# Kernel optimization log

Measured on AMD Instinct MI355X. Metric: run time of the kernel, lower is better.

## Reference

```python
import jax, jax.numpy as jnp
import numpy as np

B, H, W, C = 4, 64, 64, 512
DQK = C // 8


def setup_inputs() -> dict:
    key = jax.random.key(0)
    k1, k2, k3, k4 = jax.random.split(key, 4)
    x = jax.random.normal(k1, (B, H, W, C), dtype=jnp.float32)
    kernel_f = jax.random.normal(k2, (1, 1, C, DQK), dtype=jnp.float32) * 0.02
    kernel_g = jax.random.normal(k3, (1, 1, C, DQK), dtype=jnp.float32) * 0.02
    kernel_h = jax.random.normal(k4, (1, 1, C, C), dtype=jnp.float32) * 0.02
    gamma = jnp.ones((1,), dtype=jnp.float32)  # nonzero so attention branch contributes
    return {"x": x, "kernel_f": kernel_f, "kernel_g": kernel_g,
            "kernel_h": kernel_h, "gamma": gamma}


def reference(x, kernel_f, kernel_g, kernel_h, gamma):
    b, h, w, c = x.shape
    n = h * w
    xt = x.reshape(b, n, c)  # 1x1 conv == per-pixel matmul
    f = jnp.einsum('bnc,cd->bnd', xt, kernel_f[0, 0])       # [b,n,dqk]
    g = jnp.einsum('bnc,cd->bnd', xt, kernel_g[0, 0])       # [b,n,dqk]
    v = jnp.einsum('bnc,cd->bnd', xt, kernel_h[0, 0])       # [b,n,c]
    s = jnp.einsum('bid,bjd->bij', f, g)                    # [b,n,n] = f @ g^T
    beta = jax.nn.softmax(s, axis=-1)
    out = jnp.einsum('bij,bjc->bic', beta, v)               # [b,n,c]
    out = out.reshape(b, h, w, c)
    return gamma * out + x
```

## Files before the change

### kernel.cpp

```cpp
#include <hip/hip_runtime.h>


typedef __bf16 bf16x8 __attribute__((ext_vector_type(8)));
typedef __bf16 bf16x2 __attribute__((ext_vector_type(2)));
typedef float f32x4 __attribute__((ext_vector_type(4)));
typedef unsigned int u32x4 __attribute__((ext_vector_type(4)));
typedef unsigned int u32;

#define L2E 1.4426950408889634f

__device__ __forceinline__ unsigned short f2bf(float f) {
    unsigned int u = __builtin_bit_cast(unsigned int, f);
    u += 0x7fffu + ((u >> 16) & 1u);
    return (unsigned short)(u >> 16);
}
__device__ __forceinline__ u32 cvtpk(float a, float b) {
    bf16x2 t; t[0] = (__bf16)a; t[1] = (__bf16)b;
    return __builtin_bit_cast(u32, t);
}
__device__ __forceinline__ bf16x8 ld8(const void* p) {
    u32x4 u = *reinterpret_cast<const u32x4*>(p);
    return __builtin_bit_cast(bf16x8, u);
}
__device__ __forceinline__ bf16x8 ldx(const float* p) {
    float4 a = *reinterpret_cast<const float4*>(p);
    float4 b = *reinterpret_cast<const float4*>(p + 4);
    u32x4 r;
    r.x = cvtpk(a.x, a.y); r.y = cvtpk(a.z, a.w);
    r.z = cvtpk(b.x, b.y); r.w = cvtpk(b.z, b.w);
    return __builtin_bit_cast(bf16x8, r);
}
__device__ __forceinline__ f32x4 mfma16(bf16x8 a, bf16x8 b, f32x4 c) {
    return __builtin_amdgcn_mfma_f32_16x16x32_bf16(a, b, c, 0, 0, 0);
}
__device__ __forceinline__ void gl2lds16(const void* g, void* l) {
    __builtin_amdgcn_global_load_lds(
        (const __attribute__((address_space(1))) u32*)g,
        (__attribute__((address_space(3))) u32*)l, 16, 0, 0);
}

__global__ __launch_bounds__(256) void cvt_w_all(const float* __restrict__ kf,
                                                 const float* __restrict__ kg,
                                                 const float* __restrict__ kh,
                                                 unsigned short* __restrict__ wst) {
    int idx = blockIdx.x * 256 + threadIdx.x;
    int j = idx & 7;
    int gi = idx >> 3;
    int c = gi % 640;
    int sq = gi / 640;
    int k = (sq >> 2) * 32 + (sq & 3) * 8 + j;
    float v;
    if (c < 64)       v = kf[k * 64 + c] * L2E;
    else if (c < 128) v = kg[k * 64 + (c - 64)];
    else              v = kh[k * 512 + (c - 128)];
    wst[idx] = f2bf(v);
}

__global__ __launch_bounds__(256, 2) void proj_k(const float* __restrict__ x,
                                                 const unsigned short* __restrict__ wst,
                                                 unsigned short* __restrict__ fq,
                                                 unsigned short* __restrict__ kst,
                                                 unsigned short* __restrict__ vst) {
    __shared__ __align__(16) unsigned char Wl[2][20480];
    __shared__ unsigned short Tl[64][72];

    int m0 = blockIdx.x * 64;
    int grp = blockIdx.y;
    int tid = threadIdx.x;
    int w = tid >> 6, l = tid & 63, g = l >> 4, i = l & 15;

    const char* wsrc = (const char*)wst + (size_t)w * 10240 + (size_t)grp * 5120 + l * 16;

#pragma unroll
    for (int s5 = 0; s5 < 5; s5++)
        gl2lds16(wsrc + s5 * 1024, &Wl[0][w * 5120 + s5 * 1024]);

    const float* xrow = x + (size_t)(m0 + 16 * w + i) * 512 + g * 8;
    bf16x8 af[16];
#pragma unroll
    for (int k = 0; k < 16; k++) af[k] = ldx(xrow + 32 * k);

    f32x4 acc[5][4];
#pragma unroll
    for (int t = 0; t < 5; t++)
#pragma unroll
        for (int cf = 0; cf < 4; cf++) acc[t][cf] = f32x4{0, 0, 0, 0};

    int rdoff = g * 5120 + i * 16;

#pragma unroll
    for (int q = 0; q < 16; q++) {
        __syncthreads();
        if (q < 15) {
            const char* src = wsrc + (size_t)(q + 1) * 40960;
#pragma unroll
            for (int s5 = 0; s5 < 5; s5++)
                gl2lds16(src + s5 * 1024, &Wl[(q + 1) & 1][w * 5120 + s5 * 1024]);
        }
        const unsigned char* Wb = &Wl[q & 1][0];
        __builtin_amdgcn_s_setprio(1);
#pragma unroll
        for (int t = 0; t < 5; t++)
#pragma unroll
            for (int cf = 0; cf < 4; cf++) {
                bf16x8 bb = ld8(Wb + rdoff + (t * 64 + 16 * cf) * 16);
                acc[t][cf] = mfma16(af[q], bb, acc[t][cf]);
            }
        __builtin_amdgcn_s_setprio(0);
    }

    int batch = m0 >> 12;
    int kt = (m0 & 4095) >> 6;
    unsigned short* kbase = kst + (size_t)batch * 262144 + (size_t)kt * 4096;
    unsigned short* vbase = vst + (size_t)batch * 2097152 + (size_t)kt * 32768;

#pragma unroll
    for (int t = 0; t < 5; t++) {
        if (grp == 0 && t == 0) {
#pragma unroll
            for (int cf = 0; cf < 4; cf++)
#pragma unroll
                for (int r = 0; r < 4; r++)
                    fq[(size_t)(m0 + 16 * w + 4 * g + r) * 64 + 16 * cf + i] =
                        f2bf(acc[t][cf][r]);
        } else {
            __syncthreads();
#pragma unroll
            for (int cf = 0; cf < 4; cf++) {
                ushort4 v4;
                v4.x = f2bf(acc[t][cf][0]); v4.y = f2bf(acc[t][cf][1]);
                v4.z = f2bf(acc[t][cf][2]); v4.w = f2bf(acc[t][cf][3]);
                *reinterpret_cast<ushort4*>(&Tl[16 * cf + i][16 * w + 4 * g]) = v4;
            }
            __syncthreads();
            if (grp == 0 && t == 1) {
#pragma unroll
                for (int ch = tid; ch < 512; ch += 256) {
                    int jf2 = ch >> 7, ks = (ch >> 6) & 1, l2 = ch & 63;
                    int g2 = l2 >> 4, i2 = l2 & 15;
                    ushort4 o0, o1;
                    o0.x = Tl[ks * 32 + 8 * g2 + 0][16 * jf2 + i2];
                    o0.y = Tl[ks * 32 + 8 * g2 + 1][16 * jf2 + i2];
                    o0.z = Tl[ks * 32 + 8 * g2 + 2][16 * jf2 + i2];
                    o0.w = Tl[ks * 32 + 8 * g2 + 3][16 * jf2 + i2];
                    o1.x = Tl[ks * 32 + 8 * g2 + 4][16 * jf2 + i2];
                    o1.y = Tl[ks * 32 + 8 * g2 + 5][16 * jf2 + i2];
                    o1.z = Tl[ks * 32 + 8 * g2 + 6][16 * jf2 + i2];
                    o1.w = Tl[ks * 32 + 8 * g2 + 7][16 * jf2 + i2];
                    unsigned short* dst = kbase + (size_t)(jf2 * 1024 + ks * 512 + l2 * 8);
                    *reinterpret_cast<ushort4*>(dst)     = o0;
                    *reinterpret_cast<ushort4*>(dst + 4) = o1;
                }
            } else {
                int n0 = (grp == 0) ? (t - 2) * 64 : 192 + t * 64;
#pragma unroll
                for (int ch = tid; ch < 512; ch += 256) {
                    int cc = ch >> 7, ks = (ch >> 6) & 1, l2 = ch & 63;
                    int g2 = l2 >> 4, i2 = l2 & 15;
                    int row = cc * 16 + i2;
                    int jb = 32 * ks + 4 * g2;
                    ushort4 o0, o1;
                    o0.x = Tl[row][jb + 0];  o0.y = Tl[row][jb + 1];
                    o0.z = Tl[row][jb + 2];  o0.w = Tl[row][jb + 3];
                    o1.x = Tl[row][jb + 16]; o1.y = Tl[row][jb + 17];
                    o1.z = Tl[row][jb + 18]; o1.w = Tl[row][jb + 19];
                    int c16 = (n0 >> 4) + cc;
                    unsigned short* dst = vbase + (size_t)(c16 * 1024 + ks * 512 + l2 * 8);
                    *reinterpret_cast<ushort4*>(dst)     = o0;
                    *reinterpret_cast<ushort4*>(dst + 4) = o1;
                }
            }
        }
    }
}

__global__ __launch_bounds__(512, 2) void attn_k(const unsigned short* __restrict__ fq,
                                                 const unsigned short* __restrict__ kst,
                                                 const unsigned short* __restrict__ vst,
                                                 const float* __restrict__ x,
                                                 const float* __restrict__ gamma,
                                                 float* __restrict__ out) {
    __shared__ __align__(16) unsigned char Pl[4][8192];
    __shared__ float l_lds[64];

    int bid = blockIdx.x;
    int xcd = bid & 7;
    int batch = xcd >> 1;
    int qidx = ((xcd & 1) << 5) | (bid >> 3);
    int q0 = qidx * 64;

    int tid = threadIdx.x;
    int w = tid >> 6, l = tid & 63, g = l >> 4, i = l & 15;
    int jf = w >> 1, qfh = w & 1;

    if (tid < 64) l_lds[tid] = 0.0f;

    const unsigned short* fqb = fq + (size_t)batch * 4096 * 64;
    const char* kb = (const char*)kst + (size_t)batch * 524288;
    const char* vb = (const char*)vst + (size_t)batch * 4194304;

    bf16x8 aQ[2][2];
#pragma unroll
    for (int qf_l = 0; qf_l < 2; qf_l++)
#pragma unroll
        for (int ks = 0; ks < 2; ks++)
            aQ[qf_l][ks] = ld8(fqb + (size_t)(q0 + 16 * (2 * qfh + qf_l) + i) * 64 +
                               ks * 32 + g * 8);

    f32x4 acc[4][4];
#pragma unroll
    for (int a = 0; a < 4; a++)
#pragma unroll
        for (int b = 0; b < 4; b++) acc[a][b] = f32x4{0, 0, 0, 0};
    float lp[2] = {0.0f, 0.0f};

    int pwoff = ((2 * qfh) * 2 + (jf >> 1)) * 1024 + l * 16 + (jf & 1) * 8;
    int c16w = w * 4;
    int wpar = w & 1;

    bf16x8 kAa[2], kAb[2];
    kAa[0] = ld8(kb + (size_t)jf * 2048 + l * 16);
    kAa[1] = ld8(kb + (size_t)jf * 2048 + 1024 + l * 16);
    kAb[0] = ld8(kb + (size_t)(4 + jf) * 2048 + l * 16);
    kAb[1] = ld8(kb + (size_t)(4 + jf) * 2048 + 1024 + l * 16);

    bf16x8 vbr_a[4][2], vbr_b[4][2];
#pragma unroll
    for (int cf = 0; cf < 4; cf++)
#pragma unroll
        for (int ks = 0; ks < 2; ks++) {
            vbr_a[cf][ks] = ld8(vb + (size_t)(c16w + cf) * 2048 + ks * 1024 + l * 16);
            vbr_b[cf][ks] = ld8(vb + (size_t)(32 + c16w + cf) * 2048 + ks * 1024 + l * 16);
        }

    {
        f32x4 s0[2] = {f32x4{0,0,0,0}, f32x4{0,0,0,0}};
        f32x4 s1[2] = {f32x4{0,0,0,0}, f32x4{0,0,0,0}};
#pragma unroll
        for (int qf_l = 0; qf_l < 2; qf_l++) {
            s0[qf_l] = mfma16(kAa[0], aQ[qf_l][0], s0[qf_l]);
            s0[qf_l] = mfma16(kAa[1], aQ[qf_l][1], s0[qf_l]);
            s1[qf_l] = mfma16(kAb[0], aQ[qf_l][0], s1[qf_l]);
            s1[qf_l] = mfma16(kAb[1], aQ[qf_l][1], s1[qf_l]);
        }
        kAa[0] = ld8(kb + (size_t)(8 + jf) * 2048 + l * 16);
        kAa[1] = ld8(kb + (size_t)(8 + jf) * 2048 + 1024 + l * 16);
        kAb[0] = ld8(kb + (size_t)(12 + jf) * 2048 + l * 16);
        kAb[1] = ld8(kb + (size_t)(12 + jf) * 2048 + 1024 + l * 16);
#pragma unroll
        for (int qf_l = 0; qf_l < 2; qf_l++) {
            float p0 = __builtin_amdgcn_exp2f(s0[qf_l][0]);
            float p1 = __builtin_amdgcn_exp2f(s0[qf_l][1]);
            float p2 = __builtin_amdgcn_exp2f(s0[qf_l][2]);
            float p3 = __builtin_amdgcn_exp2f(s0[qf_l][3]);
            lp[qf_l] += (p0 + p1) + (p2 + p3);
            uint2 pk2; pk2.x = cvtpk(p0, p1); pk2.y = cvtpk(p2, p3);
            *reinterpret_cast<uint2*>(&Pl[0][0] + pwoff + qf_l * 2048) = pk2;
            p0 = __builtin_amdgcn_exp2f(s1[qf_l][0]);
            p1 = __builtin_amdgcn_exp2f(s1[qf_l][1]);
            p2 = __builtin_amdgcn_exp2f(s1[qf_l][2]);
            p3 = __builtin_amdgcn_exp2f(s1[qf_l][3]);
            lp[qf_l] += (p0 + p1) + (p2 + p3);
            pk2.x = cvtpk(p0, p1); pk2.y = cvtpk(p2, p3);
            *reinterpret_cast<uint2*>(&Pl[1][0] + pwoff + qf_l * 2048) = pk2;
        }
    }

    for (int u = 0; u < 32; ++u) {
        asm volatile("s_waitcnt lgkmcnt(0)" ::: "memory");
        __builtin_amdgcn_s_barrier();

        const unsigned char* Pr0 = &Pl[(u & 1) * 2][0];
        const unsigned char* Pr1 = Pr0 + 8192;

        f32x4 s0[2] = {f32x4{0,0,0,0}, f32x4{0,0,0,0}};
        f32x4 s1[2] = {f32x4{0,0,0,0}, f32x4{0,0,0,0}};
#pragma unroll
        for (int qf_l = 0; qf_l < 2; qf_l++) {
            s0[qf_l] = mfma16(kAa[0], aQ[qf_l][0], s0[qf_l]);
            s0[qf_l] = mfma16(kAa[1], aQ[qf_l][1], s0[qf_l]);
            s1[qf_l] = mfma16(kAb[0], aQ[qf_l][0], s1[qf_l]);
            s1[qf_l] = mfma16(kAb[1], aQ[qf_l][1], s1[qf_l]);
        }

        {
            int ta = (2 * u + 4) & 63, tb = (2 * u + 5) & 63;
            const char* ka = kb + (size_t)(ta * 4 + jf) * 2048;
            const char* kp = kb + (size_t)(tb * 4 + jf) * 2048;
            kAa[0] = ld8(ka + l * 16);
            kAa[1] = ld8(ka + 1024 + l * 16);
            kAb[0] = ld8(kp + l * 16);
            kAb[1] = ld8(kp + 1024 + l * 16);
        }

        float msk = (u < 31) ? 1.0f : 0.0f;
        unsigned char* Pw0 = &Pl[((u + 1) & 1) * 2][0];
        unsigned char* Pw1 = Pw0 + 8192;

        if (wpar == 0) {
            {
                bf16x8 aP[4][2];
#pragma unroll
                for (int qf = 0; qf < 4; qf++)
#pragma unroll
                    for (int ks = 0; ks < 2; ks++)
                        aP[qf][ks] = ld8(Pr0 + (qf * 2 + ks) * 1024 + l * 16);
                __builtin_amdgcn_s_setprio(1);
#pragma unroll
                for (int cf = 0; cf < 4; cf++)
#pragma unroll
                    for (int qf = 0; qf < 4; qf++) {
                        acc[qf][cf] = mfma16(aP[qf][0], vbr_a[cf][0], acc[qf][cf]);
                        acc[qf][cf] = mfma16(aP[qf][1], vbr_a[cf][1], acc[qf][cf]);
                    }
                __builtin_amdgcn_s_setprio(0);
            }
            {
                int tv = (2 * u + 2) & 63;
#pragma unroll
                for (int cf = 0; cf < 4; cf++)
#pragma unroll
                    for (int ks = 0; ks < 2; ks++)
                        vbr_a[cf][ks] = ld8(vb + (size_t)(tv * 32 + c16w + cf) * 2048 +
                                            ks * 1024 + l * 16);
            }
            {
                bf16x8 aP[4][2];
#pragma unroll
                for (int qf = 0; qf < 4; qf++)
#pragma unroll
                    for (int ks = 0; ks < 2; ks++)
                        aP[qf][ks] = ld8(Pr1 + (qf * 2 + ks) * 1024 + l * 16);
                __builtin_amdgcn_s_setprio(1);
#pragma unroll
                for (int cf = 0; cf < 4; cf++)
#pragma unroll
                    for (int qf = 0; qf < 4; qf++) {
                        acc[qf][cf] = mfma16(aP[qf][0], vbr_b[cf][0], acc[qf][cf]);
                        acc[qf][cf] = mfma16(aP[qf][1], vbr_b[cf][1], acc[qf][cf]);
                    }
                __builtin_amdgcn_s_setprio(0);
            }
            {
                int tv = (2 * u + 3) & 63;
#pragma unroll
                for (int cf = 0; cf < 4; cf++)
#pragma unroll
                    for (int ks = 0; ks < 2; ks++)
                        vbr_b[cf][ks] = ld8(vb + (size_t)(tv * 32 + c16w + cf) * 2048 +
                                            ks * 1024 + l * 16);
            }
#pragma unroll
            for (int qf_l = 0; qf_l < 2; qf_l++) {
                float p0 = __builtin_amdgcn_exp2f(s0[qf_l][0]);
                float p1 = __builtin_amdgcn_exp2f(s0[qf_l][1]);
                float p2 = __builtin_amdgcn_exp2f(s0[qf_l][2]);
                float p3 = __builtin_amdgcn_exp2f(s0[qf_l][3]);
                lp[qf_l] += msk * ((p0 + p1) + (p2 + p3));
                uint2 pk2; pk2.x = cvtpk(p0, p1); pk2.y = cvtpk(p2, p3);
                *reinterpret_cast<uint2*>(Pw0 + pwoff + qf_l * 2048) = pk2;
                p0 = __builtin_amdgcn_exp2f(s1[qf_l][0]);
                p1 = __builtin_amdgcn_exp2f(s1[qf_l][1]);
                p2 = __builtin_amdgcn_exp2f(s1[qf_l][2]);
                p3 = __builtin_amdgcn_exp2f(s1[qf_l][3]);
                lp[qf_l] += msk * ((p0 + p1) + (p2 + p3));
                pk2.x = cvtpk(p0, p1); pk2.y = cvtpk(p2, p3);
                *reinterpret_cast<uint2*>(Pw1 + pwoff + qf_l * 2048) = pk2;
            }
        } else {
            {
                bf16x8 aP[4][2];
#pragma unroll
                for (int qf = 0; qf < 4; qf++)
#pragma unroll
                    for (int ks = 0; ks < 2; ks++)
                        aP[qf][ks] = ld8(Pr1 + (qf * 2 + ks) * 1024 + l * 16);
                __builtin_amdgcn_s_setprio(1);
#pragma unroll
                for (int cf = 0; cf < 4; cf++)
#pragma unroll
                    for (int qf = 0; qf < 4; qf++) {
                        acc[qf][cf] = mfma16(aP[qf][0], vbr_b[cf][0], acc[qf][cf]);
                        acc[qf][cf] = mfma16(aP[qf][1], vbr_b[cf][1], acc[qf][cf]);
                    }
                __builtin_amdgcn_s_setprio(0);
            }
            {
                int tv = (2 * u + 3) & 63;
#pragma unroll
                for (int cf = 0; cf < 4; cf++)
#pragma unroll
                    for (int ks = 0; ks < 2; ks++)
                        vbr_b[cf][ks] = ld8(vb + (size_t)(tv * 32 + c16w + cf) * 2048 +
                                            ks * 1024 + l * 16);
            }
#pragma unroll
            for (int qf_l = 0; qf_l < 2; qf_l++) {
                float p0 = __builtin_amdgcn_exp2f(s0[qf_l][0]);
                float p1 = __builtin_amdgcn_exp2f(s0[qf_l][1]);
                float p2 = __builtin_amdgcn_exp2f(s0[qf_l][2]);
                float p3 = __builtin_amdgcn_exp2f(s0[qf_l][3]);
                lp[qf_l] += msk * ((p0 + p1) + (p2 + p3));
                uint2 pk2; pk2.x = cvtpk(p0, p1); pk2.y = cvtpk(p2, p3);
                *reinterpret_cast<uint2*>(Pw0 + pwoff + qf_l * 2048) = pk2;
                p0 = __builtin_amdgcn_exp2f(s1[qf_l][0]);
                p1 = __builtin_amdgcn_exp2f(s1[qf_l][1]);
                p2 = __builtin_amdgcn_exp2f(s1[qf_l][2]);
                p3 = __builtin_amdgcn_exp2f(s1[qf_l][3]);
                lp[qf_l] += msk * ((p0 + p1) + (p2 + p3));
                pk2.x = cvtpk(p0, p1); pk2.y = cvtpk(p2, p3);
                *reinterpret_cast<uint2*>(Pw1 + pwoff + qf_l * 2048) = pk2;
            }
            {
                bf16x8 aP[4][2];
#pragma unroll
                for (int qf = 0; qf < 4; qf++)
#pragma unroll
                    for (int ks = 0; ks < 2; ks++)
                        aP[qf][ks] = ld8(Pr0 + (qf * 2 + ks) * 1024 + l * 16);
                __builtin_amdgcn_s_setprio(1);
#pragma unroll
                for (int cf = 0; cf < 4; cf++)
#pragma unroll
                    for (int qf = 0; qf < 4; qf++) {
                        acc[qf][cf] = mfma16(aP[qf][0], vbr_a[cf][0], acc[qf][cf]);
                        acc[qf][cf] = mfma16(aP[qf][1], vbr_a[cf][1], acc[qf][cf]);
                    }
                __builtin_amdgcn_s_setprio(0);
            }
            {
                int tv = (2 * u + 2) & 63;
#pragma unroll
                for (int cf = 0; cf < 4; cf++)
#pragma unroll
                    for (int ks = 0; ks < 2; ks++)
                        vbr_a[cf][ks] = ld8(vb + (size_t)(tv * 32 + c16w + cf) * 2048 +
                                            ks * 1024 + l * 16);
            }
        }
    }

#pragma unroll
    for (int qf_l = 0; qf_l < 2; qf_l++) {
        lp[qf_l] += __shfl_xor(lp[qf_l], 16, 64);
        lp[qf_l] += __shfl_xor(lp[qf_l], 32, 64);
    }
    if (g == 0) {
        atomicAdd(&l_lds[16 * (2 * qfh + 0) + i], lp[0]);
        atomicAdd(&l_lds[16 * (2 * qfh + 1) + i], lp[1]);
    }
    __syncthreads();

    float gam = gamma[0];
#pragma unroll
    for (int qf = 0; qf < 4; qf++) {
#pragma unroll
        for (int r = 0; r < 4; r++) {
            float linv = gam / l_lds[16 * qf + 4 * g + r];
            int n = q0 + 16 * qf + 4 * g + r;
            size_t base = ((size_t)batch * 4096 + n) * 512 + 64 * w;
#pragma unroll
            for (int cf = 0; cf < 4; cf++)
                out[base + 16 * cf + i] = acc[qf][cf][r] * linv + x[base + 16 * cf + i];
        }
    }
}


extern "C" void kernel_launch(void* const* d_in, const int* in_sizes, int n_in,
                              void* d_out, int out_size, void* d_ws, size_t ws_size,
                              hipStream_t stream) {
    const float* x = (const float*)d_in[0];
    const float* kf = (const float*)d_in[1];
    const float* kg = (const float*)d_in[2];
    const float* kh = (const float*)d_in[3];
    const float* gamma = (const float*)d_in[4];
    float* out = (float*)d_out;

    char* ws = (char*)d_ws;
    unsigned short* Fq  = (unsigned short*)(ws);
    unsigned short* Kst = (unsigned short*)(ws + 2097152);
    unsigned short* Vst = (unsigned short*)(ws + 4194304);
    unsigned short* Wst = (unsigned short*)(ws + 20971520);

    cvt_w_all<<<1280, 256, 0, stream>>>(kf, kg, kh, Wst);
    proj_k<<<dim3(256, 2), 256, 0, stream>>>(x, Wst, Fq, Kst, Vst);
    attn_k<<<256, 512, 0, stream>>>(Fq, Kst, Vst, x, gamma, out);
}
```

Baseline: 111.6 us.

## Process four key tiles per barrier step in attention loop

The main attention loop now handles four 16-key sub-tiles per iteration instead of two, so there are half as many block barriers. The P buffer doubles to 64KB of LDS for double-buffering four tiles. The wave-parity split, in which odd waves computed exp before consuming P, is removed, so all waves follow one uniform order. The aim is to cut barrier and synchronisation overhead, at the cost of more registers for K and S fragments, more LDS (which may limit two blocks per CU), and less staggering between waves.

```diff
diff --git a/kernel.cpp b/kernel.cpp
--- a/kernel.cpp
+++ b/kernel.cpp
@@ -180,7 +180,7 @@
                                                  const float* __restrict__ x,
                                                  const float* __restrict__ gamma,
                                                  float* __restrict__ out) {
-    __shared__ __align__(16) unsigned char Pl[4][8192];
+    __shared__ __align__(16) unsigned char Pl[8][8192];
     __shared__ float l_lds[64];
 
     int bid = blockIdx.x;
@@ -216,13 +216,13 @@
 
     int pwoff = ((2 * qfh) * 2 + (jf >> 1)) * 1024 + l * 16 + (jf & 1) * 8;
     int c16w = w * 4;
-    int wpar = w & 1;
-
-    bf16x8 kAa[2], kAb[2];
-    kAa[0] = ld8(kb + (size_t)jf * 2048 + l * 16);
-    kAa[1] = ld8(kb + (size_t)jf * 2048 + 1024 + l * 16);
-    kAb[0] = ld8(kb + (size_t)(4 + jf) * 2048 + l * 16);
-    kAb[1] = ld8(kb + (size_t)(4 + jf) * 2048 + 1024 + l * 16);
+
+    bf16x8 kA[4][2];
+#pragma unroll
+    for (int t4 = 0; t4 < 4; t4++)
+#pragma unroll
+        for (int ks = 0; ks < 2; ks++)
+            kA[t4][ks] = ld8(kb + (size_t)(t4 * 4 + jf) * 2048 + ks * 1024 + l * 16);
 
     bf16x8 vbr_a[4][2], vbr_b[4][2];
 #pragma unroll
@@ -234,210 +234,186 @@
         }
 
     {
-        f32x4 s0[2] = {f32x4{0,0,0,0}, f32x4{0,0,0,0}};
-        f32x4 s1[2] = {f32x4{0,0,0,0}, f32x4{0,0,0,0}};
-#pragma unroll
-        for (int qf_l = 0; qf_l < 2; qf_l++) {
-            s0[qf_l] = mfma16(kAa[0], aQ[qf_l][0], s0[qf_l]);
-            s0[qf_l] = mfma16(kAa[1], aQ[qf_l][1], s0[qf_l]);
-            s1[qf_l] = mfma16(kAb[0], aQ[qf_l][0], s1[qf_l]);
-            s1[qf_l] = mfma16(kAb[1], aQ[qf_l][1], s1[qf_l]);
-        }
-        kAa[0] = ld8(kb + (size_t)(8 + jf) * 2048 + l * 16);
-        kAa[1] = ld8(kb + (size_t)(8 + jf) * 2048 + 1024 + l * 16);
-        kAb[0] = ld8(kb + (size_t)(12 + jf) * 2048 + l * 16);
-        kAb[1] = ld8(kb + (size_t)(12 + jf) * 2048 + 1024 + l * 16);
-#pragma unroll
-        for (int qf_l = 0; qf_l < 2; qf_l++) {
-            float p0 = __builtin_amdgcn_exp2f(s0[qf_l][0]);
-            float p1 = __builtin_amdgcn_exp2f(s0[qf_l][1]);
-            float p2 = __builtin_amdgcn_exp2f(s0[qf_l][2]);
-            float p3 = __builtin_amdgcn_exp2f(s0[qf_l][3]);
-            lp[qf_l] += (p0 + p1) + (p2 + p3);
-            uint2 pk2; pk2.x = cvtpk(p0, p1); pk2.y = cvtpk(p2, p3);
-            *reinterpret_cast<uint2*>(&Pl[0][0] + pwoff + qf_l * 2048) = pk2;
-            p0 = __builtin_amdgcn_exp2f(s1[qf_l][0]);
-            p1 = __builtin_amdgcn_exp2f(s1[qf_l][1]);
-            p2 = __builtin_amdgcn_exp2f(s1[qf_l][2]);
-            p3 = __builtin_amdgcn_exp2f(s1[qf_l][3]);
-            lp[qf_l] += (p0 + p1) + (p2 + p3);
-            pk2.x = cvtpk(p0, p1); pk2.y = cvtpk(p2, p3);
-            *reinterpret_cast<uint2*>(&Pl[1][0] + pwoff + qf_l * 2048) = pk2;
-        }
-    }
-
-    for (int u = 0; u < 32; ++u) {
+        f32x4 s[4][2];
+#pragma unroll
+        for (int t4 = 0; t4 < 4; t4++)
+#pragma unroll
+            for (int qf_l = 0; qf_l < 2; qf_l++) s[t4][qf_l] = f32x4{0, 0, 0, 0};
+#pragma unroll
+        for (int t4 = 0; t4 < 4; t4++)
+#pragma unroll
+            for (int qf_l = 0; qf_l < 2; qf_l++) {
+                s[t4][qf_l] = mfma16(kA[t4][0], aQ[qf_l][0], s[t4][qf_l]);
+                s[t4][qf_l] = mfma16(kA[t4][1], aQ[qf_l][1], s[t4][qf_l]);
+            }
+#pragma unroll
+        for (int t4 = 0; t4 < 4; t4++)
+#pragma unroll
+            for (int ks = 0; ks < 2; ks++)
+                kA[t4][ks] = ld8(kb + (size_t)((4 + t4) * 4 + jf) * 2048 + ks * 1024 + l * 16);
+#pragma unroll
+        for (int t4 = 0; t4 < 4; t4++)
+#pragma unroll
+            for (int qf_l = 0; qf_l < 2; qf_l++) {
+                float p0 = __builtin_amdgcn_exp2f(s[t4][qf_l][0]);
+                float p1 = __builtin_amdgcn_exp2f(s[t4][qf_l][1]);
+                float p2 = __builtin_amdgcn_exp2f(s[t4][qf_l][2]);
+                float p3 = __builtin_amdgcn_exp2f(s[t4][qf_l][3]);
+                lp[qf_l] += (p0 + p1) + (p2 + p3);
+                uint2 pk2; pk2.x = cvtpk(p0, p1); pk2.y = cvtpk(p2, p3);
+                *reinterpret_cast<uint2*>(&Pl[t4][0] + pwoff + qf_l * 2048) = pk2;
+            }
+    }
+
+    for (int u = 0; u < 16; ++u) {
         asm volatile("s_waitcnt lgkmcnt(0)" ::: "memory");
         __builtin_amdgcn_s_barrier();
 
-        const unsigned char* Pr0 = &Pl[(u & 1) * 2][0];
-        const unsigned char* Pr1 = Pr0 + 8192;
-
-        f32x4 s0[2] = {f32x4{0,0,0,0}, f32x4{0,0,0,0}};
-        f32x4 s1[2] = {f32x4{0,0,0,0}, f32x4{0,0,0,0}};
-#pragma unroll
-        for (int qf_l = 0; qf_l < 2; qf_l++) {
-            s0[qf_l] = mfma16(kAa[0], aQ[qf_l][0], s0[qf_l]);
-            s0[qf_l] = mfma16(kAa[1], aQ[qf_l][1], s0[qf_l]);
-            s1[qf_l] = mfma16(kAb[0], aQ[qf_l][0], s1[qf_l]);
-            s1[qf_l] = mfma16(kAb[1], aQ[qf_l][1], s1[qf_l]);
-        }
-
-        {
-            int ta = (2 * u + 4) & 63, tb = (2 * u + 5) & 63;
-            const char* ka = kb + (size_t)(ta * 4 + jf) * 2048;
-            const char* kp = kb + (size_t)(tb * 4 + jf) * 2048;
-            kAa[0] = ld8(ka + l * 16);
-            kAa[1] = ld8(ka + 1024 + l * 16);
-            kAb[0] = ld8(kp + l * 16);
-            kAb[1] = ld8(kp + 1024 + l * 16);
-        }
-
-        float msk = (u < 31) ? 1.0f : 0.0f;
-        unsigned char* Pw0 = &Pl[((u + 1) & 1) * 2][0];
-        unsigned char* Pw1 = Pw0 + 8192;
-
-        if (wpar == 0) {
-            {
-                bf16x8 aP[4][2];
-#pragma unroll
-                for (int qf = 0; qf < 4; qf++)
-#pragma unroll
-                    for (int ks = 0; ks < 2; ks++)
-                        aP[qf][ks] = ld8(Pr0 + (qf * 2 + ks) * 1024 + l * 16);
-                __builtin_amdgcn_s_setprio(1);
-#pragma unroll
-                for (int cf = 0; cf < 4; cf++)
-#pragma unroll
-                    for (int qf = 0; qf < 4; qf++) {
-                        acc[qf][cf] = mfma16(aP[qf][0], vbr_a[cf][0], acc[qf][cf]);
-                        acc[qf][cf] = mfma16(aP[qf][1], vbr_a[cf][1], acc[qf][cf]);
-                    }
-                __builtin_amdgcn_s_setprio(0);
-            }
-            {
-                int tv = (2 * u + 2) & 63;
-#pragma unroll
-                for (int cf = 0; cf < 4; cf++)
-#pragma unroll
-                    for (int ks = 0; ks < 2; ks++)
-                        vbr_a[cf][ks] = ld8(vb + (size_t)(tv * 32 + c16w + cf) * 2048 +
-                                            ks * 1024 + l * 16);
-            }
-            {
-                bf16x8 aP[4][2];
-#pragma unroll
-                for (int qf = 0; qf < 4; qf++)
-#pragma unroll
-                    for (int ks = 0; ks < 2; ks++)
-                        aP[qf][ks] = ld8(Pr1 + (qf * 2 + ks) * 1024 + l * 16);
-                __builtin_amdgcn_s_setprio(1);
-#pragma unroll
-                for (int cf = 0; cf < 4; cf++)
-#pragma unroll
-                    for (int qf = 0; qf < 4; qf++) {
-                        acc[qf][cf] = mfma16(aP[qf][0], vbr_b[cf][0], acc[qf][cf]);
-                        acc[qf][cf] = mfma16(aP[qf][1], vbr_b[cf][1], acc[qf][cf]);
-                    }
-                __builtin_amdgcn_s_setprio(0);
-            }
-            {
-                int tv = (2 * u + 3) & 63;
-#pragma unroll
-                for (int cf = 0; cf < 4; cf++)
-#pragma unroll
-                    for (int ks = 0; ks < 2; ks++)
-                        vbr_b[cf][ks] = ld8(vb + (size_t)(tv * 32 + c16w + cf) * 2048 +
-                                            ks * 1024 + l * 16);
-            }
+        const unsigned char* Prq = &Pl[(u & 1) * 4][0];
+
+        f32x4 s[4][2];
+#pragma unroll
+        for (int t4 = 0; t4 < 4; t4++)
+#pragma unroll
+            for (int qf_l = 0; qf_l < 2; qf_l++) s[t4][qf_l] = f32x4{0, 0, 0, 0};
+#pragma unroll
+        for (int t4 = 0; t4 < 4; t4++)
 #pragma unroll
             for (int qf_l = 0; qf_l < 2; qf_l++) {
-                float p0 = __builtin_amdgcn_exp2f(s0[qf_l][0]);
-                float p1 = __builtin_amdgcn_exp2f(s0[qf_l][1]);
-                float p2 = __builtin_amdgcn_exp2f(s0[qf_l][2]);
-                float p3 = __builtin_amdgcn_exp2f(s0[qf_l][3]);
+                s[t4][qf_l] = mfma16(kA[t4][0], aQ[qf_l][0], s[t4][qf_l]);
+                s[t4][qf_l] = mfma16(kA[t4][1], aQ[qf_l][1], s[t4][qf_l]);
+            }
+
+#pragma unroll
+        for (int t4 = 0; t4 < 4; t4++) {
+            int tk = (4 * u + 8 + t4) & 63;
+#pragma unroll
+            for (int ks = 0; ks < 2; ks++)
+                kA[t4][ks] = ld8(kb + (size_t)(tk * 4 + jf) * 2048 + ks * 1024 + l * 16);
+        }
+
+        {
+            bf16x8 aP[4][2];
+#pragma unroll
+            for (int qf = 0; qf < 4; qf++)
+#pragma unroll
+                for (int ks = 0; ks < 2; ks++)
+                    aP[qf][ks] = ld8(Prq + (qf * 2 + ks) * 1024 + l * 16);
+            __builtin_amdgcn_s_setprio(1);
+#pragma unroll
+            for (int cf = 0; cf < 4; cf++)
+#pragma unroll
+                for (int qf = 0; qf < 4; qf++) {
+                    acc[qf][cf] = mfma16(aP[qf][0], vbr_a[cf][0], acc[qf][cf]);
+                    acc[qf][cf] = mfma16(aP[qf][1], vbr_a[cf][1], acc[qf][cf]);
+                }
+            __builtin_amdgcn_s_setprio(0);
+        }
+        {
+            int tv = (4 * u + 2) & 63;
+#pragma unroll
+            for (int cf = 0; cf < 4; cf++)
+#pragma unroll
+                for (int ks = 0; ks < 2; ks++)
+                    vbr_a[cf][ks] = ld8(vb + (size_t)(tv * 32 + c16w + cf) * 2048 +
+                                        ks * 1024 + l * 16);
+        }
+
+        {
+            bf16x8 aP[4][2];
+#pragma unroll
+            for (int qf = 0; qf < 4; qf++)
+#pragma unroll
+                for (int ks = 0; ks < 2; ks++)
+                    aP[qf][ks] = ld8(Prq + 8192 + (qf * 2 + ks) * 1024 + l * 16);
+            __builtin_amdgcn_s_setprio(1);
+#pragma unroll
+            for (int cf = 0; cf < 4; cf++)
+#pragma unroll
+                for (int qf = 0; qf < 4; qf++) {
+                    acc[qf][cf] = mfma16(aP[qf][0], vbr_b[cf][0], acc[qf][cf]);
+                    acc[qf][cf] = mfma16(aP[qf][1], vbr_b[cf][1], acc[qf][cf]);
+                }
+            __builtin_amdgcn_s_setprio(0);
+        }
+        {
+            int tv = (4 * u + 3) & 63;
+#pragma unroll
+            for (int cf = 0; cf < 4; cf++)
+#pragma unroll
+                for (int ks = 0; ks < 2; ks++)
+                    vbr_b[cf][ks] = ld8(vb + (size_t)(tv * 32 + c16w + cf) * 2048 +
+                                        ks * 1024 + l * 16);
+        }
+
+        {
+            bf16x8 aP[4][2];
+#pragma unroll
+            for (int qf = 0; qf < 4; qf++)
+#pragma unroll
+                for (int ks = 0; ks < 2; ks++)
+                    aP[qf][ks] = ld8(Prq + 16384 + (qf * 2 + ks) * 1024 + l * 16);
+            __builtin_amdgcn_s_setprio(1);
+#pragma unroll
+            for (int cf = 0; cf < 4; cf++)
+#pragma unroll
+                for (int qf = 0; qf < 4; qf++) {
+                    acc[qf][cf] = mfma16(aP[qf][0], vbr_a[cf][0], acc[qf][cf]);
+                    acc[qf][cf] = mfma16(aP[qf][1], vbr_a[cf][1], acc[qf][cf]);
+                }
+            __builtin_amdgcn_s_setprio(0);
+        }
+        {
+            int tv = (4 * u + 4) & 63;
+#pragma unroll
+            for (int cf = 0; cf < 4; cf++)
+#pragma unroll
+                for (int ks = 0; ks < 2; ks++)
+                    vbr_a[cf][ks] = ld8(vb + (size_t)(tv * 32 + c16w + cf) * 2048 +
+                                        ks * 1024 + l * 16);
+        }
+
+        {
+            bf16x8 aP[4][2];
+#pragma unroll
+            for (int qf = 0; qf < 4; qf++)
+#pragma unroll
+                for (int ks = 0; ks < 2; ks++)
+                    aP[qf][ks] = ld8(Prq + 24576 + (qf * 2 + ks) * 1024 + l * 16);
+            __builtin_amdgcn_s_setprio(1);
+#pragma unroll
+            for (int cf = 0; cf < 4; cf++)
+#pragma unroll
+                for (int qf = 0; qf < 4; qf++) {
+                    acc[qf][cf] = mfma16(aP[qf][0], vbr_b[cf][0], acc[qf][cf]);
+                    acc[qf][cf] = mfma16(aP[qf][1], vbr_b[cf][1], acc[qf][cf]);
+                }
+            __builtin_amdgcn_s_setprio(0);
+        }
+        {
+            int tv = (4 * u + 5) & 63;
+#pragma unroll
+            for (int cf = 0; cf < 4; cf++)
+#pragma unroll
+                for (int ks = 0; ks < 2; ks++)
+                    vbr_b[cf][ks] = ld8(vb + (size_t)(tv * 32 + c16w + cf) * 2048 +
+                                        ks * 1024 + l * 16);
+        }
+
+        float msk = (u < 15) ? 1.0f : 0.0f;
+        unsigned char* Pwq = &Pl[((u + 1) & 1) * 4][0];
+#pragma unroll
+        for (int t4 = 0; t4 < 4; t4++)
+#pragma unroll
+            for (int qf_l = 0; qf_l < 2; qf_l++) {
+                float p0 = __builtin_amdgcn_exp2f(s[t4][qf_l][0]);
+                float p1 = __builtin_amdgcn_exp2f(s[t4][qf_l][1]);
+                float p2 = __builtin_amdgcn_exp2f(s[t4][qf_l][2]);
+                float p3 = __builtin_amdgcn_exp2f(s[t4][qf_l][3]);
                 lp[qf_l] += msk * ((p0 + p1) + (p2 + p3));
                 uint2 pk2; pk2.x = cvtpk(p0, p1); pk2.y = cvtpk(p2, p3);
-                *reinterpret_cast<uint2*>(Pw0 + pwoff + qf_l * 2048) = pk2;
-                p0 = __builtin_amdgcn_exp2f(s1[qf_l][0]);
-                p1 = __builtin_amdgcn_exp2f(s1[qf_l][1]);
-                p2 = __builtin_amdgcn_exp2f(s1[qf_l][2]);
-                p3 = __builtin_amdgcn_exp2f(s1[qf_l][3]);
-                lp[qf_l] += msk * ((p0 + p1) + (p2 + p3));
-                pk2.x = cvtpk(p0, p1); pk2.y = cvtpk(p2, p3);
-                *reinterpret_cast<uint2*>(Pw1 + pwoff + qf_l * 2048) = pk2;
-            }
-        } else {
-            {
-                bf16x8 aP[4][2];
-#pragma unroll
-                for (int qf = 0; qf < 4; qf++)
-#pragma unroll
-                    for (int ks = 0; ks < 2; ks++)
-                        aP[qf][ks] = ld8(Pr1 + (qf * 2 + ks) * 1024 + l * 16);
-                __builtin_amdgcn_s_setprio(1);
-#pragma unroll
-                for (int cf = 0; cf < 4; cf++)
-#pragma unroll
-                    for (int qf = 0; qf < 4; qf++) {
-                        acc[qf][cf] = mfma16(aP[qf][0], vbr_b[cf][0], acc[qf][cf]);
-                        acc[qf][cf] = mfma16(aP[qf][1], vbr_b[cf][1], acc[qf][cf]);
-                    }
-                __builtin_amdgcn_s_setprio(0);
-            }
-            {
-                int tv = (2 * u + 3) & 63;
-#pragma unroll
-                for (int cf = 0; cf < 4; cf++)
-#pragma unroll
-                    for (int ks = 0; ks < 2; ks++)
-                        vbr_b[cf][ks] = ld8(vb + (size_t)(tv * 32 + c16w + cf) * 2048 +
-                                            ks * 1024 + l * 16);
-            }
-#pragma unroll
-            for (int qf_l = 0; qf_l < 2; qf_l++) {
-                float p0 = __builtin_amdgcn_exp2f(s0[qf_l][0]);
-                float p1 = __builtin_amdgcn_exp2f(s0[qf_l][1]);
-                float p2 = __builtin_amdgcn_exp2f(s0[qf_l][2]);
-                float p3 = __builtin_amdgcn_exp2f(s0[qf_l][3]);
-                lp[qf_l] += msk * ((p0 + p1) + (p2 + p3));
-                uint2 pk2; pk2.x = cvtpk(p0, p1); pk2.y = cvtpk(p2, p3);
-                *reinterpret_cast<uint2*>(Pw0 + pwoff + qf_l * 2048) = pk2;
-                p0 = __builtin_amdgcn_exp2f(s1[qf_l][0]);
-                p1 = __builtin_amdgcn_exp2f(s1[qf_l][1]);
-                p2 = __builtin_amdgcn_exp2f(s1[qf_l][2]);
-                p3 = __builtin_amdgcn_exp2f(s1[qf_l][3]);
-                lp[qf_l] += msk * ((p0 + p1) + (p2 + p3));
-                pk2.x = cvtpk(p0, p1); pk2.y = cvtpk(p2, p3);
-                *reinterpret_cast<uint2*>(Pw1 + pwoff + qf_l * 2048) = pk2;
-            }
-            {
-                bf16x8 aP[4][2];
-#pragma unroll
-                for (int qf = 0; qf < 4; qf++)
-#pragma unroll
-                    for (int ks = 0; ks < 2; ks++)
-                        aP[qf][ks] = ld8(Pr0 + (qf * 2 + ks) * 1024 + l * 16);
-                __builtin_amdgcn_s_setprio(1);
-#pragma unroll
-                for (int cf = 0; cf < 4; cf++)
-#pragma unroll
-                    for (int qf = 0; qf < 4; qf++) {
-                        acc[qf][cf] = mfma16(aP[qf][0], vbr_a[cf][0], acc[qf][cf]);
-                        acc[qf][cf] = mfma16(aP[qf][1], vbr_a[cf][1], acc[qf][cf]);
-                    }
-                __builtin_amdgcn_s_setprio(0);
-            }
-            {
-                int tv = (2 * u + 2) & 63;
-#pragma unroll
-                for (int cf = 0; cf < 4; cf++)
-#pragma unroll
-                    for (int ks = 0; ks < 2; ks++)
-                        vbr_a[cf][ks] = ld8(vb + (size_t)(tv * 32 + c16w + cf) * 2048 +
-                                            ks * 1024 + l * 16);
-            }
-        }
+                *reinterpret_cast<uint2*>(Pwq + t4 * 8192 + pwoff + qf_l * 2048) = pk2;
+            }
     }
 
 #pragma unroll
```

Result: slower. 128.0 us (+14.7%).
